# Optimization experiments

Measured on AMD Instinct MI355X. Metric: run time of the kernel, lower is better.

## Reference

```python
import jax, jax.numpy as jnp
import numpy as np

N, E, IN_DIM, OUT_DIM, R = 50000, 800000, 128, 128, 8


def setup_inputs() -> dict:
    key = jax.random.key(0)
    k1, k2, k3, k4, k5 = jax.random.split(key, 5)
    x = jax.random.normal(k1, (N, IN_DIM), dtype=jnp.float32)
    edge_index = jax.random.randint(k2, (2, E), 0, N, dtype=jnp.int32)
    edge_type = jax.random.randint(k3, (E,), 0, R, dtype=jnp.int32)
    # Xavier-uniform-ish init for parameters
    lim_w = float(np.sqrt(6.0 / (IN_DIM + OUT_DIM)))
    weight = jax.random.uniform(k4, (R, IN_DIM, OUT_DIM), dtype=jnp.float32, minval=-lim_w, maxval=lim_w)
    self_weight = jax.random.uniform(k5, (IN_DIM, OUT_DIM), dtype=jnp.float32, minval=-lim_w, maxval=lim_w)
    return {"x": x, "weight": weight, "self_weight": self_weight,
            "edge_index": edge_index, "edge_type": edge_type}


def reference(x, weight, self_weight, edge_index, edge_type):
    n = x.shape[0]
    r = weight.shape[0]
    d_out = weight.shape[2]
    src, dst = edge_index[0], edge_index[1]
    # undirected: symmetrize edges (directed=False)
    src_all = jnp.concatenate([src, dst])          # [2E]
    dst_all = jnp.concatenate([dst, src])          # [2E]
    et_all = jnp.concatenate([edge_type, edge_type])  # [2E]
    # transform all nodes by every relation weight once: [R, N, D_out]
    xw = jnp.einsum('ni,rio->rno', x, weight)
    # gather per-edge messages already transformed by their relation's W_r
    msg = xw[et_all, src_all]                      # [2E, D_out]
    # fused (relation, dst) segment id -> per-relation scatter-add
    seg = et_all.astype(jnp.int32) * n + dst_all
    agg = jax.ops.segment_sum(msg, seg, num_segments=r * n).reshape(r, n, d_out)
    deg = jax.ops.segment_sum(jnp.ones_like(seg, dtype=x.dtype), seg,
                              num_segments=r * n).reshape(r, n)
    deg_inv = jnp.where(deg > 0, 1.0 / jnp.maximum(deg, 1.0), jnp.zeros_like(deg))
    out = jnp.sum(agg * deg_inv[..., None], axis=0)  # [N, D_out]
    out = out + x @ self_weight                       # self-loop
    return out
```

## Files before the change

### kernel.cpp

```cpp
#include <hip/hip_runtime.h>

#define NN 50000
#define EE 800000
#define RR 8
#define DD 128
#define SS (NN*RR)
#define TE (2*EE)
#define NB 782
#define NBLK 391
#define NS (NB*NBLK)
#define CONVB 6826
#define XWB 391

typedef __attribute__((ext_vector_type(8))) short bf16x8;
typedef __attribute__((ext_vector_type(4))) float f32x4;

__device__ __forceinline__ unsigned short f2bf(float f){
  unsigned int u = __float_as_uint(f);
  u += 0x7fffu + ((u >> 16) & 1u);
  return (unsigned short)(u >> 16);
}
__device__ __forceinline__ float bf_lo(unsigned int w){ return __uint_as_float(w << 16); }
__device__ __forceinline__ float bf_hi(unsigned int w){ return __uint_as_float(w & 0xffff0000u); }

__device__ __forceinline__ void acc8(float* a, uint4 u){
  a[0] += bf_lo(u.x); a[1] += bf_hi(u.x);
  a[2] += bf_lo(u.y); a[3] += bf_hi(u.y);
  a[4] += bf_lo(u.z); a[5] += bf_hi(u.z);
  a[6] += bf_lo(u.w); a[7] += bf_hi(u.w);
}
__device__ __forceinline__ void acc8s(float* a, uint4 u, float s){
  a[0] += s*bf_lo(u.x); a[1] += s*bf_hi(u.x);
  a[2] += s*bf_lo(u.y); a[3] += s*bf_hi(u.y);
  a[4] += s*bf_lo(u.z); a[5] += s*bf_hi(u.z);
  a[6] += s*bf_lo(u.w); a[7] += s*bf_hi(u.w);
}

__device__ __forceinline__ void dir_edge(const int* ei, const int* et, int j,
                                         int& s, int& d, int& t){
  if (j < EE){ s = ei[j]; d = ei[EE + j]; t = et[j]; }
  else { int jj = j - EE; s = ei[EE + jj]; d = ei[jj]; t = et[jj]; }
}

__global__ __launch_bounds__(256) void k_histconv(
    const int* __restrict__ ei, const int* __restrict__ et,
    int* __restrict__ hist,
    const float* __restrict__ x, const float* __restrict__ w,
    const float* __restrict__ sw,
    unsigned short* __restrict__ xb, unsigned short* __restrict__ wb)
{
  __shared__ int h[NB];
  if (blockIdx.x < NBLK){
    int tid = threadIdx.x, bid = blockIdx.x;
    for (int i = tid; i < NB; i += 256) h[i] = 0;
    __syncthreads();
    int j0 = bid*4096;
    for (int k = tid; k < 4096; k += 256){
      int j = j0 + k;
      if (j < TE){
        int s, d, t; dir_edge(ei, et, j, s, d, t);
        atomicAdd(&h[d >> 6], 1);
      }
    }
    __syncthreads();
    for (int i = tid; i < NB; i += 256) hist[i*NBLK + bid] = h[i];
  } else {
    int i = (blockIdx.x - NBLK)*256 + threadIdx.x;
    const int M1 = NN*DD/4;
    if (i < M1){
      float4 v = ((const float4*)x)[i];
      ushort4 o;
      o.x = f2bf(v.x); o.y = f2bf(v.y); o.z = f2bf(v.z); o.w = f2bf(v.w);
      ((ushort4*)xb)[i] = o;
    } else {
      int j = i - M1;
      if (j < 9*DD*DD){
        int r = j >> 14; int rem = j & 16383; int n = rem >> 7; int k = rem & 127;
        float v = (r < 8) ? w[r*16384 + k*128 + n] : sw[k*128 + n];
        wb[j] = f2bf(v);
      }
    }
  }
}

__global__ __launch_bounds__(256) void k_scan1(int* __restrict__ hist,
                                               int* __restrict__ blksum){
  __shared__ int sd[256];
  int b = blockIdx.x, tid = threadIdx.x;
  int base = b*1024 + tid*4;
  int v0 = (base+0 < NS) ? hist[base+0] : 0;
  int v1 = (base+1 < NS) ? hist[base+1] : 0;
  int v2 = (base+2 < NS) ? hist[base+2] : 0;
  int v3 = (base+3 < NS) ? hist[base+3] : 0;
  int ts = v0+v1+v2+v3;
  sd[tid] = ts; __syncthreads();
  for (int o = 1; o < 256; o <<= 1){
    int t = (tid >= o) ? sd[tid-o] : 0;
    __syncthreads();
    sd[tid] += t;
    __syncthreads();
  }
  int ex = sd[tid] - ts;
  if (base+0 < NS) hist[base+0] = ex; ex += v0;
  if (base+1 < NS) hist[base+1] = ex; ex += v1;
  if (base+2 < NS) hist[base+2] = ex; ex += v2;
  if (base+3 < NS) hist[base+3] = ex;
  if (tid == 255) blksum[b] = sd[255];
}

__global__ __launch_bounds__(512) void k_scan2(int* __restrict__ blksum, int nb){
  __shared__ int sd[512];
  int tid = threadIdx.x;
  int v = (tid < nb) ? blksum[tid] : 0;
  sd[tid] = v; __syncthreads();
  for (int o = 1; o < 512; o <<= 1){
    int t = (tid >= o) ? sd[tid-o] : 0;
    __syncthreads();
    sd[tid] += t;
    __syncthreads();
  }
  if (tid < nb) blksum[tid] = sd[tid] - v;
}

__global__ __launch_bounds__(256) void k_scan3(int* __restrict__ hist,
                                               const int* __restrict__ blksum){
  int i = blockIdx.x*blockDim.x + threadIdx.x;
  if (i < NS) hist[i] += blksum[i >> 10];
}

__global__ __launch_bounds__(256, 2) void k_partxw(
    const int* __restrict__ ei, const int* __restrict__ et,
    const int* __restrict__ S, unsigned int* __restrict__ P,
    const unsigned short* __restrict__ xb,
    const unsigned short* __restrict__ wb,
    unsigned short* __restrict__ xw)
{
  __shared__ __align__(16) unsigned short Bs[2][16384];
  if (blockIdx.x < NBLK){
    int* cur = (int*)&Bs[0][0];
    int tid = threadIdx.x, bid = blockIdx.x;
    for (int i = tid; i < NB; i += 256) cur[i] = S[i*NBLK + bid];
    __syncthreads();
    int j0 = bid*4096;
    for (int k = tid; k < 4096; k += 256){
      int j = j0 + k;
      if (j < TE){
        int s, d, t; dir_edge(ei, et, j, s, d, t);
        int b = d >> 6;
        int p = atomicAdd(&cur[b], 1);
        P[p] = (unsigned int)s | ((unsigned int)(d & 63) << 17)
             | ((unsigned int)t << 23);
      }
    }
  } else {
    const int bid  = blockIdx.x - NBLK;
    const int tid  = threadIdx.x;
    const int wave = tid >> 6, lane = tid & 63;
    const int l15  = lane & 15, quad = lane >> 4;
    const int row0 = bid * 128 + wave * 32;

    bf16x8 af[2][4];
    #pragma unroll
    for (int m = 0; m < 2; ++m){
      int gr = row0 + m*16 + l15; if (gr >= NN) gr = NN - 1;
      #pragma unroll
      for (int ks = 0; ks < 4; ++ks)
        af[m][ks] = *(const bf16x8*)(xb + (size_t)gr*DD + ks*32 + quad*8);
    }

    auto stage = [&](int r, int b){
      #pragma unroll
      for (int j = 0; j < 8; ++j){
        int n = j*16 + wave*4 + (lane >> 4);
        int c = lane & 15;
        const unsigned short* gp = wb + r*16384 + n*128 + ((c ^ (n & 7)) << 3);
        __builtin_amdgcn_global_load_lds(
            (const __attribute__((address_space(1))) void*)gp,
            (__attribute__((address_space(3))) void*)((char*)&Bs[b][0] + j*4096 + wave*1024),
            16, 0, 0);
      }
    };

    stage(0, 0);

    #pragma unroll 1
    for (int r = 0; r < 9; ++r){
      __syncthreads();
      if (r < 8) stage(r + 1, (r + 1) & 1);

      f32x4 C[2][8];
      #pragma unroll
      for (int m = 0; m < 2; ++m)
        #pragma unroll
        for (int nt = 0; nt < 8; ++nt) C[m][nt] = (f32x4)(0.f);

      const char* bb = (const char*)&Bs[r & 1][0];
      #pragma unroll
      for (int nt = 0; nt < 8; ++nt){
        bf16x8 bf[4];
        #pragma unroll
        for (int ks = 0; ks < 4; ++ks)
          bf[ks] = *(const bf16x8*)(bb + (nt*16 + l15)*256
                                       + (((ks*4 + quad) ^ (l15 & 7)) << 4));
        #pragma unroll
        for (int ks = 0; ks < 4; ++ks){
          C[0][nt] = __builtin_amdgcn_mfma_f32_16x16x32_bf16(af[0][ks], bf[ks], C[0][nt], 0, 0, 0);
          C[1][nt] = __builtin_amdgcn_mfma_f32_16x16x32_bf16(af[1][ks], bf[ks], C[1][nt], 0, 0, 0);
        }
      }

      unsigned short* xs = xw + (size_t)r * NN * DD;
      #pragma unroll
      for (int m = 0; m < 2; ++m)
        #pragma unroll
        for (int nt = 0; nt < 8; ++nt)
          #pragma unroll
          for (int i = 0; i < 4; ++i){
            int gr = row0 + m*16 + quad*4 + i;
            if (gr < NN) xs[(size_t)gr*DD + nt*16 + l15] = f2bf(C[m][nt][i]);
          }
    }
  }
}

__global__ __launch_bounds__(256) void k_build(const unsigned int* __restrict__ P,
                                               const int* __restrict__ S,
                                               int* __restrict__ esrc,
                                               int* __restrict__ offs){
  __shared__ int h[512], cu[512], sd[256];
  int tid = threadIdx.x, b = blockIdx.x;
  int pstart = S[b*NBLK];
  int pend   = (b+1 < NB) ? S[(b+1)*NBLK] : TE;
  int ne = pend - pstart;
  h[2*tid] = 0; h[2*tid+1] = 0;
  __syncthreads();
  for (int k = tid; k < ne; k += 256){
    unsigned int u = P[pstart + k];
    int lseg = (int)(((u >> 17) & 63u)*8u + (u >> 23));
    atomicAdd(&h[lseg], 1);
  }
  __syncthreads();
  int v0 = h[2*tid], v1 = h[2*tid+1];
  int ts = v0 + v1;
  sd[tid] = ts; __syncthreads();
  for (int o = 1; o < 256; o <<= 1){
    int t = (tid >= o) ? sd[tid-o] : 0;
    __syncthreads();
    sd[tid] += t;
    __syncthreads();
  }
  int ex = sd[tid] - ts;
  cu[2*tid]   = pstart + ex;
  cu[2*tid+1] = pstart + ex + v0;
  int seg0 = b*512;
  if (seg0 + 2*tid     < SS) offs[seg0 + 2*tid]     = cu[2*tid];
  if (seg0 + 2*tid + 1 < SS) offs[seg0 + 2*tid + 1] = cu[2*tid+1];
  if (b == NB-1 && tid == 0) offs[SS] = TE;
  __syncthreads();
  for (int k = tid; k < ne; k += 256){
    unsigned int u = P[pstart + k];
    int lseg = (int)(((u >> 17) & 63u)*8u + (u >> 23));
    int r = atomicAdd(&cu[lseg], 1);
    esrc[r] = (int)(u & 0x1ffffu) | (int)(((u >> 23) & 7u) << 17);
  }
}

__global__ __launch_bounds__(256, 4) void k_agg(
    const unsigned short* __restrict__ xw,
    const int* __restrict__ offs,
    const int* __restrict__ esrc,
    float* __restrict__ out)
{
  const int tid   = threadIdx.x;
  const int lane  = tid & 63;
  const int gl    = lane & 15;
  const int basel = lane & 48;
  const int d     = blockIdx.x * 16 + (tid >> 4);

  int o = 0;
  if (gl < 9) o = offs[d*8 + gl];
  int onx = __shfl(o, (basel + gl + 1) & 63);
  int cnt = onx - o;
  float scale = (gl < 8 && cnt > 0) ? 1.0f/(float)cnt : 0.0f;
  int ebase = __shfl(o, basel);
  int etot  = __shfl(o, basel + 8) - ebase;

  float a[8] = {0.f,0.f,0.f,0.f,0.f,0.f,0.f,0.f};

  int pk[8];
  #pragma unroll
  for (int s = 0; s < 8; ++s) pk[s] = (s < etot) ? esrc[ebase + s] : 0;

  for (int e = 0; e < etot; e += 8){
    uint4 U[8]; float sc[8];
    #pragma unroll
    for (int s = 0; s < 8; ++s){
      sc[s] = 0.f;
      U[s] = make_uint4(0u,0u,0u,0u);
      if (e + s < etot){
        int rel = (pk[s] >> 17) & 7;
        sc[s]   = __shfl(scale, basel + rel);
        int src = pk[s] & 0x1ffff;
        U[s] = *(const uint4*)(xw + ((size_t)rel*NN + src)*DD + gl*8);
      }
    }
    #pragma unroll
    for (int s = 0; s < 8; ++s){
      int en = e + 8 + s;
      pk[s] = (en < etot) ? esrc[ebase + en] : 0;
    }
    #pragma unroll
    for (int s = 0; s < 8; ++s) acc8s(a, U[s], sc[s]);
  }

  {
    uint4 u = *(const uint4*)(xw + ((size_t)8*NN + d)*DD + gl*8);
    acc8(a, u);
  }

  float4 v0; v0.x = a[0]; v0.y = a[1]; v0.z = a[2]; v0.w = a[3];
  float4 v1; v1.x = a[4]; v1.y = a[5]; v1.z = a[6]; v1.w = a[7];
  *(float4*)(out + (size_t)d*DD + gl*8)     = v0;
  *(float4*)(out + (size_t)d*DD + gl*8 + 4) = v1;
}

extern "C" void kernel_launch(void* const* d_in, const int* in_sizes, int n_in,
                              void* d_out, int out_size, void* d_ws, size_t ws_size,
                              hipStream_t stream){
  const float* x  = (const float*)d_in[0];
  const float* w  = (const float*)d_in[1];
  const float* sw = (const float*)d_in[2];
  const int*   ei = (const int*)d_in[3];
  const int*   et = (const int*)d_in[4];
  float* out = (float*)d_out;
  char* ws = (char*)d_ws;

  if (ws_size < (size_t)136295168) return;

  unsigned short* xb = (unsigned short*)(ws + 0);
  int*          esrc = (int*)(ws + 12800000);
  int*          offs = (int*)(ws + 19200000);
  unsigned short* wb = (unsigned short*)(ws + 20800016);
  unsigned short* xw = (unsigned short*)(ws + 21095168);

  unsigned int*    P = (unsigned int*)((char*)d_out + 0);
  int*          hist = (int*)((char*)d_out + 6400000);
  int*        blksum = (int*)((char*)d_out + 7623168);

  k_histconv<<<NBLK + CONVB, 256, 0, stream>>>(ei, et, hist, x, w, sw, xb, wb);
  k_scan1<<<(NS + 1023)/1024, 256, 0, stream>>>(hist, blksum);
  k_scan2<<<1, 512, 0, stream>>>(blksum, (NS + 1023)/1024);
  k_scan3<<<(NS + 255)/256, 256, 0, stream>>>(hist, blksum);
  k_partxw<<<NBLK + XWB, 256, 0, stream>>>(ei, et, hist, P, xb, wb, xw);
  k_build<<<NB, 256, 0, stream>>>(P, hist, esrc, offs);
  k_agg<<<NN/16, 256, 0, stream>>>(xw, offs, esrc, out);
}
```

Measured before the change: 241.5 us.

## Stage relation weights in quarter tiles to shrink LDS and raise occupancy

The fused partition/XW kernel now stages each relation's 128x128 bf16 weight in four 32-column quarters with double buffering, instead of whole 32 KB tiles. This cuts LDS per block from 64 KB to 16 KB and drops the 16 live accumulator vectors to two per step, so launch bounds go from 2 to 5 blocks per CU. It adds more barriers and an explicit vmcnt drain per quarter, which may hurt overlap. The aggregation kernel's launch bound is also raised from 4 to 8 to push occupancy there as well.

```diff
diff --git a/kernel.cpp b/kernel.cpp
--- a/kernel.cpp
+++ b/kernel.cpp
@@ -14,6 +14,11 @@
 
 typedef __attribute__((ext_vector_type(8))) short bf16x8;
 typedef __attribute__((ext_vector_type(4))) float f32x4;
+
+#define DRAIN_VM do { \
+    asm volatile("s_waitcnt vmcnt(0)" ::: "memory"); \
+    __builtin_amdgcn_sched_barrier(0); \
+  } while (0)
 
 __device__ __forceinline__ unsigned short f2bf(float f){
   unsigned int u = __float_as_uint(f);
@@ -128,14 +133,14 @@
   if (i < NS) hist[i] += blksum[i >> 10];
 }
 
-__global__ __launch_bounds__(256, 2) void k_partxw(
+__global__ __launch_bounds__(256, 5) void k_partxw(
     const int* __restrict__ ei, const int* __restrict__ et,
     const int* __restrict__ S, unsigned int* __restrict__ P,
     const unsigned short* __restrict__ xb,
     const unsigned short* __restrict__ wb,
     unsigned short* __restrict__ xw)
 {
-  __shared__ __align__(16) unsigned short Bs[2][16384];
+  __shared__ __align__(16) unsigned short Bs[2][4096];
   if (blockIdx.x < NBLK){
     int* cur = (int*)&Bs[0][0];
     int tid = threadIdx.x, bid = blockIdx.x;
@@ -168,57 +173,57 @@
         af[m][ks] = *(const bf16x8*)(xb + (size_t)gr*DD + ks*32 + quad*8);
     }
 
-    auto stage = [&](int r, int b){
+    auto stage = [&](int rr, int qq, int bfb){
       #pragma unroll
-      for (int j = 0; j < 8; ++j){
-        int n = j*16 + wave*4 + (lane >> 4);
+      for (int j = 0; j < 2; ++j){
+        int rowq = (wave*2 + j)*4 + (lane >> 4);
+        int n = qq*32 + rowq;
         int c = lane & 15;
-        const unsigned short* gp = wb + r*16384 + n*128 + ((c ^ (n & 7)) << 3);
+        const unsigned short* gp = wb + rr*16384 + n*128 + ((c ^ (n & 7)) << 3);
         __builtin_amdgcn_global_load_lds(
             (const __attribute__((address_space(1))) void*)gp,
-            (__attribute__((address_space(3))) void*)((char*)&Bs[b][0] + j*4096 + wave*1024),
+            (__attribute__((address_space(3))) void*)((char*)&Bs[bfb][0] + (wave*2 + j)*1024),
             16, 0, 0);
       }
     };
 
-    stage(0, 0);
+    stage(0, 0, 0);
 
     #pragma unroll 1
     for (int r = 0; r < 9; ++r){
-      __syncthreads();
-      if (r < 8) stage(r + 1, (r + 1) & 1);
-
-      f32x4 C[2][8];
-      #pragma unroll
-      for (int m = 0; m < 2; ++m)
-        #pragma unroll
-        for (int nt = 0; nt < 8; ++nt) C[m][nt] = (f32x4)(0.f);
-
-      const char* bb = (const char*)&Bs[r & 1][0];
-      #pragma unroll
-      for (int nt = 0; nt < 8; ++nt){
-        bf16x8 bf[4];
-        #pragma unroll
-        for (int ks = 0; ks < 4; ++ks)
-          bf[ks] = *(const bf16x8*)(bb + (nt*16 + l15)*256
-                                       + (((ks*4 + quad) ^ (l15 & 7)) << 4));
-        #pragma unroll
-        for (int ks = 0; ks < 4; ++ks){
-          C[0][nt] = __builtin_amdgcn_mfma_f32_16x16x32_bf16(af[0][ks], bf[ks], C[0][nt], 0, 0, 0);
-          C[1][nt] = __builtin_amdgcn_mfma_f32_16x16x32_bf16(af[1][ks], bf[ks], C[1][nt], 0, 0, 0);
-        }
-      }
-
       unsigned short* xs = xw + (size_t)r * NN * DD;
       #pragma unroll
-      for (int m = 0; m < 2; ++m)
+      for (int q = 0; q < 4; ++q){
+        DRAIN_VM;
+        __syncthreads();
+        {
+          int nqq = r*4 + q + 1;
+          if (nqq < 36) stage(nqq >> 2, nqq & 3, (q + 1) & 1);
+        }
+        const char* bb = (const char*)&Bs[q & 1][0];
         #pragma unroll
-        for (int nt = 0; nt < 8; ++nt)
+        for (int lnt = 0; lnt < 2; ++lnt){
+          int nt = q*2 + lnt;
+          bf16x8 bf4[4];
+          #pragma unroll
+          for (int ks = 0; ks < 4; ++ks)
+            bf4[ks] = *(const bf16x8*)(bb + (lnt*16 + l15)*256
+                                          + (((ks*4 + quad) ^ (l15 & 7)) << 4));
+          f32x4 C0 = (f32x4)(0.f), C1 = (f32x4)(0.f);
+          #pragma unroll
+          for (int ks = 0; ks < 4; ++ks){
+            C0 = __builtin_amdgcn_mfma_f32_16x16x32_bf16(af[0][ks], bf4[ks], C0, 0, 0, 0);
+            C1 = __builtin_amdgcn_mfma_f32_16x16x32_bf16(af[1][ks], bf4[ks], C1, 0, 0, 0);
+          }
           #pragma unroll
           for (int i = 0; i < 4; ++i){
-            int gr = row0 + m*16 + quad*4 + i;
-            if (gr < NN) xs[(size_t)gr*DD + nt*16 + l15] = f2bf(C[m][nt][i]);
+            int gr0 = row0 + quad*4 + i;
+            int gr1 = row0 + 16 + quad*4 + i;
+            if (gr0 < NN) xs[(size_t)gr0*DD + nt*16 + l15] = f2bf(C0[i]);
+            if (gr1 < NN) xs[(size_t)gr1*DD + nt*16 + l15] = f2bf(C1[i]);
           }
+        }
+      }
     }
   }
 }
@@ -265,7 +270,7 @@
   }
 }
 
-__global__ __launch_bounds__(256, 4) void k_agg(
+__global__ __launch_bounds__(256, 8) void k_agg(
     const unsigned short* __restrict__ xw,
     const int* __restrict__ offs,
     const int* __restrict__ esrc,
```

Measured after the change: 307.5 us. 1.27x slower.
